# Kernel tuning notes

Measured on AMD Instinct MI355X. Metric: run time of the kernel, lower is better.

The kernel has to match this reference:

```python
import jax, jax.numpy as jnp
import numpy as np

B, S, D = 8, 4096, 1024

def setup_inputs() -> dict:
    key = jax.random.key(0)
    ks = jax.random.split(key, 5)
    scale = 1.0 / np.sqrt(D)
    x = jax.random.normal(ks[0], (B, S, D), dtype=jnp.float32)
    Wq = jax.random.normal(ks[1], (D, D), dtype=jnp.float32) * scale
    Wk = jax.random.normal(ks[2], (D, D), dtype=jnp.float32) * scale
    Wv = jax.random.normal(ks[3], (D, D), dtype=jnp.float32) * scale
    Wp = jax.random.normal(ks[4], (D, D), dtype=jnp.float32) * scale
    bp = jnp.zeros((D,), dtype=jnp.float32)
    return {"x": x, "Wq": Wq, "Wk": Wk, "Wv": Wv, "Wp": Wp, "bp": bp}

def reference(x, Wq, Wk, Wv, Wp, bp):
    # torch nn.Linear(no bias): y = x @ W^T
    q = jnp.einsum('bsd,ed->bse', x, Wq)
    k = jnp.einsum('bsd,ed->bse', x, Wk)
    v = jnp.einsum('bsd,ed->bse', x, Wv)
    # Linear attention (no softmax): (Q K^T) V == Q (K^T V), use associative order
    kv = jnp.einsum('bse,bsf->bef', k, v)       # [B, D, D]
    z = jnp.einsum('bse,bef->bsf', q, kv)       # [B, S, D]
    out = jnp.einsum('bsf,gf->bsg', z, Wp) + bp + x
    return out
```

## Files before the change

### kernel.cpp

```cpp
#include <hip/hip_runtime.h>
#include <hip/hip_bf16.h>


#define B_DIM 8
#define S_DIM 4096
#define D_DIM 1024
#define M_TOT (B_DIM * S_DIM)

using short8 = __attribute__((ext_vector_type(8))) short;
using f32x4  = __attribute__((ext_vector_type(4))) float;

#define TILE_M 128
#define TILE_N 128
#define TILE_K 64

__device__ __forceinline__ void g2l16(const void* g, void* l) {
  __builtin_amdgcn_global_load_lds(
      (const __attribute__((address_space(1))) unsigned int*)g,
      (__attribute__((address_space(3))) unsigned int*)l, 16, 0, 0);
}

__device__ __forceinline__ unsigned short f2b(float f) {
  __hip_bfloat16 h = __float2bfloat16(f);
  return __builtin_bit_cast(unsigned short, h);
}

template<bool FINAL>
__global__ __launch_bounds__(256, 3)
void gemm_bt(const unsigned short* __restrict__ A,
             const unsigned short* __restrict__ Bt,
             void* __restrict__ C,
             int K, int lda, int ldb, int ldc,
             long long sA, long long sB, long long sC,
             const float* __restrict__ bias,
             const float* __restrict__ resid)
{
  __shared__ __align__(16) unsigned short smem[TILE_M * TILE_K + TILE_N * TILE_K];
  unsigned short* As = smem;
  unsigned short* Bs = smem + TILE_M * TILE_K;

  const int tid  = threadIdx.x;
  const int wave = tid >> 6;
  const int lane = tid & 63;
  const int qd   = lane >> 4;
  const int ln   = lane & 15;
  const int wr   = (wave >> 1) * 64;
  const int wc   = (wave & 1) * 64;

  const int flat = blockIdx.y * gridDim.x + blockIdx.x;
  const int strp = flat & 7;
  const int t8   = flat >> 3;
  const int bx   = t8 % gridDim.x;
  const int by   = strp * (gridDim.y >> 3) + t8 / gridDim.x;

  const long long m0 = (long long)by * TILE_M;
  const long long n0 = (long long)bx * TILE_N;
  const int bz = blockIdx.z;

  const unsigned short* Ab = A  + (long long)bz * sA;
  const unsigned short* Bb = Bt + (long long)bz * sB;

  const int srow = tid >> 3;
  const int scg  = ((tid & 7) + (tid >> 3)) & 7;
  const unsigned short* pA = Ab + (m0 + srow) * lda + scg * 8;
  const unsigned short* pB = Bb + (n0 + srow) * ldb + scg * 8;
  const long long rsA = 32LL * lda, rsB = 32LL * ldb;
  unsigned short* lA = As + wave * 512;
  unsigned short* lB = Bs + wave * 512;

  int rowA[4], sA0[4], rowB[4], sB0[4];
#pragma unroll
  for (int i = 0; i < 4; ++i) {
    int ra = wr + i * 16 + ln;
    int rb = wc + i * 16 + ln;
    rowA[i] = ra * 64;  sA0[i] = (qd - ra) & 7;
    rowB[i] = rb * 64;  sB0[i] = (qd - rb) & 7;
  }

  f32x4 acc[4][4];
#pragma unroll
  for (int i = 0; i < 4; ++i)
#pragma unroll
    for (int j = 0; j < 4; ++j)
      acc[i][j] = (f32x4){0.f, 0.f, 0.f, 0.f};

  for (int k0 = 0; k0 < K; k0 += TILE_K) {
#pragma unroll
    for (int it = 0; it < 4; ++it) g2l16(pA + it * rsA, lA + it * 2048);
#pragma unroll
    for (int it = 0; it < 4; ++it) g2l16(pB + it * rsB, lB + it * 2048);
    __syncthreads();

#pragma unroll
    for (int kk = 0; kk < 2; ++kk) {
      short8 af[4], bf[4];
#pragma unroll
      for (int i = 0; i < 4; ++i)
        af[i] = *(const short8*)(As + rowA[i] + (((sA0[i] + kk * 4) & 7) << 3));
#pragma unroll
      for (int j = 0; j < 4; ++j)
        bf[j] = *(const short8*)(Bs + rowB[j] + (((sB0[j] + kk * 4) & 7) << 3));
#pragma unroll
      for (int i = 0; i < 4; ++i)
#pragma unroll
        for (int j = 0; j < 4; ++j)
          acc[i][j] = __builtin_amdgcn_mfma_f32_16x16x32_bf16(af[i], bf[j], acc[i][j], 0, 0, 0);
    }
    __syncthreads();
    pA += TILE_K; pB += TILE_K;
  }

  float* Ct = (float*)smem;
  const int fr = tid >> 3;
  const int fc = (tid & 7) * 4;
  const int hr = tid >> 4;
  const int hc = (tid & 15) * 4;

#pragma unroll
  for (int p = 0; p < 4; ++p) {
    __syncthreads();
    if ((wr >> 6) == (p >> 1)) {
      const int ibase = (p & 1) * 2;
#pragma unroll
      for (int ii = 0; ii < 2; ++ii)
#pragma unroll
        for (int j = 0; j < 4; ++j)
#pragma unroll
          for (int r = 0; r < 4; ++r)
            Ct[(ii * 16 + qd * 4 + r) * 132 + wc + j * 16 + ln] = acc[ibase + ii][j][r];
    }
    __syncthreads();

    if constexpr (FINAL) {
      float* Cf = (float*)C + (long long)bz * sC;
      const float* Rf = resid + (long long)bz * sC;
      const long long grow = m0 + p * 32 + fr;
#pragma unroll
      for (int s = 0; s < 4; ++s) {
        const int c = fc + s * 32;
        float4 v = *(const float4*)(Ct + fr * 132 + c);
        const float4 bb = *(const float4*)(bias + n0 + c);
        const float4 rr = *(const float4*)(Rf + grow * ldc + n0 + c);
        v.x += bb.x + rr.x; v.y += bb.y + rr.y;
        v.z += bb.z + rr.z; v.w += bb.w + rr.w;
        *(float4*)(Cf + grow * ldc + n0 + c) = v;
      }
    } else {
      unsigned short* Cb = (unsigned short*)C + (long long)bz * sC;
#pragma unroll
      for (int rs = 0; rs < 2; ++rs) {
        const int row = hr + rs * 16;
        const long long grow = m0 + p * 32 + row;
#pragma unroll
        for (int s = 0; s < 2; ++s) {
          const int c = hc + s * 64;
          float4 v = *(const float4*)(Ct + row * 132 + c);
          ushort4 u;
          u.x = f2b(v.x); u.y = f2b(v.y); u.z = f2b(v.z); u.w = f2b(v.w);
          *(ushort4*)(Cb + grow * ldc + n0 + c) = u;
        }
      }
    }
  }
}

__global__ __launch_bounds__(256)
void transpose_bds(const unsigned short* __restrict__ src,
                   unsigned short* __restrict__ dst)
{
  __shared__ unsigned short tile[64][68];
  const int b  = blockIdx.z;
  const int s0 = blockIdx.x * 64;
  const int e0 = blockIdx.y * 64;
  const int tx = threadIdx.x & 15;
  const int ty = threadIdx.x >> 4;

#pragma unroll
  for (int r = 0; r < 4; ++r) {
    int s = ty * 4 + r;
    ushort4 d = *(const ushort4*)(src + ((size_t)b * S_DIM + s0 + s) * D_DIM + e0 + tx * 4);
    *(ushort4*)&tile[s][tx * 4] = d;
  }
  __syncthreads();
#pragma unroll
  for (int r = 0; r < 4; ++r) {
    int e = ty * 4 + r;
    ushort4 d;
    d.x = tile[tx * 4 + 0][e];
    d.y = tile[tx * 4 + 1][e];
    d.z = tile[tx * 4 + 2][e];
    d.w = tile[tx * 4 + 3][e];
    *(ushort4*)(dst + ((size_t)b * D_DIM + e0 + e) * S_DIM + s0 + tx * 4) = d;
  }
}

__global__ __launch_bounds__(256)
void cast_transpose_1k(const float* __restrict__ src, unsigned short* __restrict__ dst)
{
  __shared__ unsigned short tile[64][68];
  const int e0 = blockIdx.x * 64;
  const int d0 = blockIdx.y * 64;
  const int tx = threadIdx.x & 15;
  const int ty = threadIdx.x >> 4;

#pragma unroll
  for (int r = 0; r < 4; ++r) {
    int e = ty * 4 + r;
    float4 f = *(const float4*)(src + (size_t)(e0 + e) * D_DIM + d0 + tx * 4);
    ushort4 u;
    u.x = f2b(f.x); u.y = f2b(f.y); u.z = f2b(f.z); u.w = f2b(f.w);
    *(ushort4*)&tile[e][tx * 4] = u;
  }
  __syncthreads();
#pragma unroll
  for (int r = 0; r < 4; ++r) {
    int d = ty * 4 + r;
    ushort4 o;
    o.x = tile[tx * 4 + 0][d];
    o.y = tile[tx * 4 + 1][d];
    o.z = tile[tx * 4 + 2][d];
    o.w = tile[tx * 4 + 3][d];
    *(ushort4*)(dst + (size_t)(d0 + d) * D_DIM + e0 + tx * 4) = o;
  }
}

__global__ __launch_bounds__(256)
void cast_f32_bf16(const float* __restrict__ src, unsigned short* __restrict__ dst, int n4)
{
  int i = blockIdx.x * 256 + threadIdx.x;
  if (i >= n4) return;
  float4 f = ((const float4*)src)[i];
  ushort4 u;
  u.x = f2b(f.x); u.y = f2b(f.y); u.z = f2b(f.z); u.w = f2b(f.w);
  ((ushort4*)dst)[i] = u;
}

extern "C" void kernel_launch(void* const* d_in, const int* in_sizes, int n_in,
                              void* d_out, int out_size, void* d_ws, size_t ws_size,
                              hipStream_t stream) {
  const float* x  = (const float*)d_in[0];
  const float* Wq = (const float*)d_in[1];
  const float* Wk = (const float*)d_in[2];
  const float* Wv = (const float*)d_in[3];
  const float* Wp = (const float*)d_in[4];
  const float* bp = (const float*)d_in[5];
  float* out = (float*)d_out;
  char* ws = (char*)d_ws;

  unsigned short* xb   = (unsigned short*)(ws + 0);
  unsigned short* Wpb  = (unsigned short*)(ws + 67108864);
  unsigned short* WvTb = (unsigned short*)(ws + 69206016);
  unsigned short* WqTb = (unsigned short*)(ws + 71303168);
  unsigned short* WkTb = (unsigned short*)(ws + 73400320);
  unsigned short* P1   = (unsigned short*)(ws + 75497472);
  unsigned short* P2T  = (unsigned short*)(ws + 77594624);
  unsigned short* xT   = (unsigned short*)(ws + 79691776);
  unsigned short* G    = (unsigned short*)(ws + 146800640);
  unsigned short* T    = (unsigned short*)(ws + 163577856);
  unsigned short* ET   = (unsigned short*)(ws + 180355072);

  const long long DD = (long long)D_DIM * D_DIM;
  const long long SD = (long long)S_DIM * D_DIM;

  cast_f32_bf16<<<dim3(M_TOT * D_DIM / 4 / 256), 256, 0, stream>>>(x, xb, M_TOT * D_DIM / 4);
  cast_f32_bf16<<<dim3(D_DIM * D_DIM / 4 / 256), 256, 0, stream>>>(Wp, Wpb, D_DIM * D_DIM / 4);
  cast_transpose_1k<<<dim3(16, 16), 256, 0, stream>>>(Wv, WvTb);
  cast_transpose_1k<<<dim3(16, 16), 256, 0, stream>>>(Wq, WqTb);
  cast_transpose_1k<<<dim3(16, 16), 256, 0, stream>>>(Wk, WkTb);

  dim3 gt(S_DIM / 64, D_DIM / 64, B_DIM);
  transpose_bds<<<gt, 256, 0, stream>>>(xb, xT);

  dim3 gw(D_DIM / TILE_N, D_DIM / TILE_M, 1);
  gemm_bt<false><<<gw, 256, 0, stream>>>(Wpb, WvTb, P1, D_DIM, D_DIM, D_DIM, D_DIM,
                                         0, 0, 0, nullptr, nullptr);

  gemm_bt<false><<<gw, 256, 0, stream>>>(WqTb, WkTb, P2T, D_DIM, D_DIM, D_DIM, D_DIM,
                                         0, 0, 0, nullptr, nullptr);

  dim3 g1k(D_DIM / TILE_N, D_DIM / TILE_M, B_DIM);
  gemm_bt<false><<<g1k, 256, 0, stream>>>(xT, xT, G, S_DIM, S_DIM, S_DIM, D_DIM,
                                          SD, SD, DD, nullptr, nullptr);

  gemm_bt<false><<<g1k, 256, 0, stream>>>(P1, G, T, D_DIM, D_DIM, D_DIM, D_DIM,
                                          0, DD, DD, nullptr, nullptr);

  gemm_bt<false><<<g1k, 256, 0, stream>>>(T, P2T, ET, D_DIM, D_DIM, D_DIM, D_DIM,
                                          DD, 0, DD, nullptr, nullptr);

  dim3 gf(D_DIM / TILE_N, S_DIM / TILE_M, B_DIM);
  gemm_bt<true><<<gf, 256, 0, stream>>>(xb, ET, out, D_DIM, D_DIM, D_DIM, D_DIM,
                                        SD, DD, SD, bp, x);
  (void)in_sizes; (void)n_in; (void)out_size; (void)ws_size;
}
```

Before: 520.5 us.

## Exploit Gram symmetry, fold residual into identity, fuse casts and batch weight GEMMs

The x^T x Gram GEMM now computes only the upper-triangular 128x128 tiles (36 of 64 per batch), and a small mirror kernel copies them into the lower triangle. The residual add is folded into the final GEMM by adding the identity to the diagonal of ET, so the final epilogue no longer reads the fp32 x. The x cast and transpose are fused into one pass, the three weight cast-transposes become one launch, and the two weight-product GEMMs are batched via a reordered workspace layout. This cuts FLOPs, memory traffic and launch count, but the residual now passes through bf16 and is less precise.

```diff
diff --git a/kernel.cpp b/kernel.cpp
--- a/kernel.cpp
+++ b/kernel.cpp
@@ -25,15 +25,18 @@
   return __builtin_bit_cast(unsigned short, h);
 }
 
-template<bool FINAL>
+__device__ __forceinline__ float b2f(unsigned short u) {
+  return __bfloat162float(__builtin_bit_cast(__hip_bfloat16, u));
+}
+
+template<bool FINAL, bool SYMM>
 __global__ __launch_bounds__(256, 3)
 void gemm_bt(const unsigned short* __restrict__ A,
              const unsigned short* __restrict__ Bt,
              void* __restrict__ C,
              int K, int lda, int ldb, int ldc,
              long long sA, long long sB, long long sC,
-             const float* __restrict__ bias,
-             const float* __restrict__ resid)
+             const float* __restrict__ bias)
 {
   __shared__ __align__(16) unsigned short smem[TILE_M * TILE_K + TILE_N * TILE_K];
   unsigned short* As = smem;
@@ -47,11 +50,18 @@
   const int wr   = (wave >> 1) * 64;
   const int wc   = (wave & 1) * 64;
 
-  const int flat = blockIdx.y * gridDim.x + blockIdx.x;
-  const int strp = flat & 7;
-  const int t8   = flat >> 3;
-  const int bx   = t8 % gridDim.x;
-  const int by   = strp * (gridDim.y >> 3) + t8 / gridDim.x;
+  int bx, by;
+  if constexpr (SYMM) {
+    int r = blockIdx.x, row = 0;
+    while (r >= 8 - row) { r -= 8 - row; ++row; }
+    by = row; bx = row + r;
+  } else {
+    const int flat = blockIdx.y * gridDim.x + blockIdx.x;
+    const int strp = flat & 7;
+    const int t8   = flat >> 3;
+    bx = t8 % gridDim.x;
+    by = strp * (gridDim.y >> 3) + t8 / gridDim.x;
+  }
 
   const long long m0 = (long long)by * TILE_M;
   const long long n0 = (long long)bx * TILE_N;
@@ -133,16 +143,13 @@
 
     if constexpr (FINAL) {
       float* Cf = (float*)C + (long long)bz * sC;
-      const float* Rf = resid + (long long)bz * sC;
       const long long grow = m0 + p * 32 + fr;
 #pragma unroll
       for (int s = 0; s < 4; ++s) {
         const int c = fc + s * 32;
         float4 v = *(const float4*)(Ct + fr * 132 + c);
         const float4 bb = *(const float4*)(bias + n0 + c);
-        const float4 rr = *(const float4*)(Rf + grow * ldc + n0 + c);
-        v.x += bb.x + rr.x; v.y += bb.y + rr.y;
-        v.z += bb.z + rr.z; v.w += bb.w + rr.w;
+        v.x += bb.x; v.y += bb.y; v.z += bb.z; v.w += bb.w;
         *(float4*)(Cf + grow * ldc + n0 + c) = v;
       }
     } else {
@@ -165,8 +172,49 @@
 }
 
 __global__ __launch_bounds__(256)
-void transpose_bds(const unsigned short* __restrict__ src,
-                   unsigned short* __restrict__ dst)
+void mirror_sym(unsigned short* __restrict__ G)
+{
+  __shared__ unsigned short tile[64][68];
+  int p = blockIdx.x, i = 1;
+  while (p >= i) { p -= i; ++i; }
+  const int j = p;
+  const int dr0 = i * 128 + (blockIdx.y >> 1) * 64;
+  const int dc0 = j * 128 + (blockIdx.y & 1) * 64;
+  unsigned short* Gb = G + (size_t)blockIdx.z * D_DIM * D_DIM;
+  const int tx = threadIdx.x & 15;
+  const int ty = threadIdx.x >> 4;
+
+#pragma unroll
+  for (int r = 0; r < 4; ++r) {
+    int row = ty * 4 + r;
+    ushort4 d = *(const ushort4*)(Gb + (size_t)(dc0 + row) * D_DIM + dr0 + tx * 4);
+    *(ushort4*)&tile[row][tx * 4] = d;
+  }
+  __syncthreads();
+#pragma unroll
+  for (int r = 0; r < 4; ++r) {
+    int row = ty * 4 + r;
+    ushort4 d;
+    d.x = tile[tx * 4 + 0][row];
+    d.y = tile[tx * 4 + 1][row];
+    d.z = tile[tx * 4 + 2][row];
+    d.w = tile[tx * 4 + 3][row];
+    *(ushort4*)(Gb + (size_t)(dr0 + row) * D_DIM + dc0 + tx * 4) = d;
+  }
+}
+
+__global__ __launch_bounds__(256)
+void add_eye(unsigned short* __restrict__ ET)
+{
+  const int d = blockIdx.x * 256 + threadIdx.x;
+  const size_t idx = (size_t)blockIdx.y * D_DIM * D_DIM + (size_t)d * D_DIM + d;
+  ET[idx] = f2b(b2f(ET[idx]) + 1.0f);
+}
+
+__global__ __launch_bounds__(256)
+void cast_transpose_x(const float* __restrict__ x,
+                      unsigned short* __restrict__ xb,
+                      unsigned short* __restrict__ xT)
 {
   __shared__ unsigned short tile[64][68];
   const int b  = blockIdx.z;
@@ -178,8 +226,12 @@
 #pragma unroll
   for (int r = 0; r < 4; ++r) {
     int s = ty * 4 + r;
-    ushort4 d = *(const ushort4*)(src + ((size_t)b * S_DIM + s0 + s) * D_DIM + e0 + tx * 4);
-    *(ushort4*)&tile[s][tx * 4] = d;
+    const size_t off = ((size_t)b * S_DIM + s0 + s) * D_DIM + e0 + tx * 4;
+    float4 f = *(const float4*)(x + off);
+    ushort4 u;
+    u.x = f2b(f.x); u.y = f2b(f.y); u.z = f2b(f.z); u.w = f2b(f.w);
+    *(ushort4*)&tile[s][tx * 4] = u;
+    *(ushort4*)(xb + off) = u;
   }
   __syncthreads();
 #pragma unroll
@@ -190,14 +242,20 @@
     d.y = tile[tx * 4 + 1][e];
     d.z = tile[tx * 4 + 2][e];
     d.w = tile[tx * 4 + 3][e];
-    *(ushort4*)(dst + ((size_t)b * D_DIM + e0 + e) * S_DIM + s0 + tx * 4) = d;
-  }
-}
-
-__global__ __launch_bounds__(256)
-void cast_transpose_1k(const float* __restrict__ src, unsigned short* __restrict__ dst)
+    *(ushort4*)(xT + ((size_t)b * D_DIM + e0 + e) * S_DIM + s0 + tx * 4) = d;
+  }
+}
+
+__global__ __launch_bounds__(256)
+void cast_transpose_w(const float* __restrict__ Wq, const float* __restrict__ Wk,
+                      const float* __restrict__ Wv,
+                      unsigned short* __restrict__ WqT, unsigned short* __restrict__ WkT,
+                      unsigned short* __restrict__ WvT)
 {
   __shared__ unsigned short tile[64][68];
+  const int z = blockIdx.z;
+  const float* src = (z == 0) ? Wq : (z == 1) ? Wk : Wv;
+  unsigned short* dst = (z == 0) ? WqT : (z == 1) ? WkT : WvT;
   const int e0 = blockIdx.x * 64;
   const int d0 = blockIdx.y * 64;
   const int tx = threadIdx.x & 15;
@@ -249,8 +307,8 @@
 
   unsigned short* xb   = (unsigned short*)(ws + 0);
   unsigned short* Wpb  = (unsigned short*)(ws + 67108864);
-  unsigned short* WvTb = (unsigned short*)(ws + 69206016);
-  unsigned short* WqTb = (unsigned short*)(ws + 71303168);
+  unsigned short* WqTb = (unsigned short*)(ws + 69206016);
+  unsigned short* WvTb = (unsigned short*)(ws + 71303168);
   unsigned short* WkTb = (unsigned short*)(ws + 73400320);
   unsigned short* P1   = (unsigned short*)(ws + 75497472);
   unsigned short* P2T  = (unsigned short*)(ws + 77594624);
@@ -262,34 +320,31 @@
   const long long DD = (long long)D_DIM * D_DIM;
   const long long SD = (long long)S_DIM * D_DIM;
 
-  cast_f32_bf16<<<dim3(M_TOT * D_DIM / 4 / 256), 256, 0, stream>>>(x, xb, M_TOT * D_DIM / 4);
+  dim3 gx(S_DIM / 64, D_DIM / 64, B_DIM);
+  cast_transpose_x<<<gx, 256, 0, stream>>>(x, xb, xT);
+
   cast_f32_bf16<<<dim3(D_DIM * D_DIM / 4 / 256), 256, 0, stream>>>(Wp, Wpb, D_DIM * D_DIM / 4);
-  cast_transpose_1k<<<dim3(16, 16), 256, 0, stream>>>(Wv, WvTb);
-  cast_transpose_1k<<<dim3(16, 16), 256, 0, stream>>>(Wq, WqTb);
-  cast_transpose_1k<<<dim3(16, 16), 256, 0, stream>>>(Wk, WkTb);
-
-  dim3 gt(S_DIM / 64, D_DIM / 64, B_DIM);
-  transpose_bds<<<gt, 256, 0, stream>>>(xb, xT);
-
-  dim3 gw(D_DIM / TILE_N, D_DIM / TILE_M, 1);
-  gemm_bt<false><<<gw, 256, 0, stream>>>(Wpb, WvTb, P1, D_DIM, D_DIM, D_DIM, D_DIM,
-                                         0, 0, 0, nullptr, nullptr);
-
-  gemm_bt<false><<<gw, 256, 0, stream>>>(WqTb, WkTb, P2T, D_DIM, D_DIM, D_DIM, D_DIM,
-                                         0, 0, 0, nullptr, nullptr);
+  cast_transpose_w<<<dim3(16, 16, 3), 256, 0, stream>>>(Wq, Wk, Wv, WqTb, WkTb, WvTb);
+
+  dim3 gw(D_DIM / TILE_N, D_DIM / TILE_M, 2);
+  gemm_bt<false, false><<<gw, 256, 0, stream>>>(Wpb, WvTb, P1, D_DIM, D_DIM, D_DIM, D_DIM,
+                                                DD, DD, DD, nullptr);
+
+  gemm_bt<false, true><<<dim3(36, 1, B_DIM), 256, 0, stream>>>(
+      xT, xT, G, S_DIM, S_DIM, S_DIM, D_DIM, SD, SD, DD, nullptr);
+  mirror_sym<<<dim3(28, 4, B_DIM), 256, 0, stream>>>(G);
 
   dim3 g1k(D_DIM / TILE_N, D_DIM / TILE_M, B_DIM);
-  gemm_bt<false><<<g1k, 256, 0, stream>>>(xT, xT, G, S_DIM, S_DIM, S_DIM, D_DIM,
-                                          SD, SD, DD, nullptr, nullptr);
-
-  gemm_bt<false><<<g1k, 256, 0, stream>>>(P1, G, T, D_DIM, D_DIM, D_DIM, D_DIM,
-                                          0, DD, DD, nullptr, nullptr);
-
-  gemm_bt<false><<<g1k, 256, 0, stream>>>(T, P2T, ET, D_DIM, D_DIM, D_DIM, D_DIM,
-                                          DD, 0, DD, nullptr, nullptr);
+  gemm_bt<false, false><<<g1k, 256, 0, stream>>>(P1, G, T, D_DIM, D_DIM, D_DIM, D_DIM,
+                                                 0, DD, DD, nullptr);
+
+  gemm_bt<false, false><<<g1k, 256, 0, stream>>>(T, P2T, ET, D_DIM, D_DIM, D_DIM, D_DIM,
+                                                 DD, 0, DD, nullptr);
+
+  add_eye<<<dim3(D_DIM / 256, B_DIM), 256, 0, stream>>>(ET);
 
   dim3 gf(D_DIM / TILE_N, S_DIM / TILE_M, B_DIM);
-  gemm_bt<true><<<gf, 256, 0, stream>>>(xb, ET, out, D_DIM, D_DIM, D_DIM, D_DIM,
-                                        SD, DD, SD, bp, x);
+  gemm_bt<true, false><<<gf, 256, 0, stream>>>(xb, ET, out, D_DIM, D_DIM, D_DIM, D_DIM,
+                                               SD, DD, SD, bp);
   (void)in_sizes; (void)n_in; (void)out_size; (void)ws_size;
 }
```

New measurement: 493.4 us. -5.2%, faster.
